# Kernel optimization log

Hardware: AMD Instinct MI355X
Metric: run time of the kernel (lower is better)

## Reference

```python
import jax, jax.numpy as jnp
import numpy as np

N_NODES = 100_000
N_EDGES = 3_200_000
HID = 64


def _glorot(key, shape):
    fan_in, fan_out = shape
    lim = np.sqrt(6.0 / (fan_in + fan_out)).astype(np.float32)
    return jax.random.uniform(key, shape, jnp.float32, -lim, lim)


def setup_inputs() -> dict:
    key = jax.random.key(0)
    ks = jax.random.split(key, 9)
    inp = {
        "vertex_features": jax.random.normal(ks[0], (N_NODES, 6), jnp.float32),
        "edges": jax.random.randint(ks[1], (2, N_EDGES), 0, N_NODES, dtype=jnp.int32),
        "weights": jax.random.uniform(ks[2], (N_EDGES,), jnp.float32),
    }
    dims = [(6, HID), (HID, HID), (HID, HID), (HID, HID), (HID, 1)]
    for i, (din, dout) in enumerate(dims):
        inp[f"W{i+1}"] = _glorot(ks[3 + i], (din, dout))
        inp[f"b{i+1}"] = jnp.zeros((dout,), jnp.float32)
    return inp


def reference(vertex_features, edges, weights, W1, b1, W2, b2, W3, b3, W4, b4, W5, b5):
    n = vertex_features.shape[0]
    row, col = edges[0], edges[1]
    # gcn_norm: add self-loops (weight 1.0), symmetric normalization.
    loop = jnp.arange(n, dtype=edges.dtype)
    row_f = jnp.concatenate([row, loop])   # source nodes
    col_f = jnp.concatenate([col, loop])   # target nodes (aggregation index)
    w_f = jnp.concatenate([weights, jnp.ones((n,), weights.dtype)])
    deg = jax.ops.segment_sum(w_f, col_f, num_segments=n)
    dinv = jnp.where(deg > 0, jax.lax.rsqrt(deg), jnp.zeros_like(deg))
    norm = dinv[row_f] * w_f * dinv[col_f]  # [E+N]

    x = vertex_features
    for W, b in ((W1, b1), (W2, b2), (W3, b3), (W4, b4), (W5, b5)):
        h = x @ W                              # [N, dout]
        msg = h[row_f] * norm[:, None]         # gather + scale, [E+N, dout]
        agg = jax.ops.segment_sum(msg, col_f, num_segments=n)  # scatter-add
        x = jax.nn.sigmoid(agg + b)
    # global_mean_pool with batch=None -> mean over all nodes, shape [1, 1]
    return jnp.mean(x, axis=0, keepdims=True)
```

## Files before the change

### kernel.cpp

```cpp
#include <hip/hip_runtime.h>
#include <hip/hip_fp16.h>
#include <math.h>


__device__ __forceinline__ float sigf(float x) { return 1.0f / (1.0f + expf(-x)); }

__device__ __forceinline__ float2 bf8x2_to_float2(unsigned short v) {
  unsigned int h2 = ((unsigned int)(v & 0xff00u) << 16) | ((unsigned int)(v & 0x00ffu) << 8);
  __half2 h = *reinterpret_cast<__half2*>(&h2);
  return __half22float2(h);
}

__device__ __forceinline__ float q12f(unsigned int q) {
  unsigned short hb = (unsigned short)(q << 3);
  __half h = *reinterpret_cast<__half*>(&hb);
  return __half2float(h);
}

#define RMASK 0xFFFFF
#define SUBS 8
#define TILE_SHIFT 12
#define TILE (1 << TILE_SHIFT)
#define NBMAX 512

__global__ __launch_bounds__(256) void k_count(const int* __restrict__ col,
                                               int* __restrict__ gcnt,
                                               int* __restrict__ gtile, int E, int NB) {
  __shared__ int lc[NBMAX];
  int t = threadIdx.x;
  for (int i = t; i < NB; i += 256) lc[i] = 0;
  __syncthreads();
  int base = blockIdx.x << TILE_SHIFT;
  int sub = blockIdx.x & (SUBS - 1);
  int hi = base + TILE; if (hi > E) hi = E;
  for (int e = base + t; e < hi; e += 256) atomicAdd(&lc[col[e] >> 8], 1);
  __syncthreads();
  size_t gt = (size_t)blockIdx.x * NB;
  for (int i = t; i < NB; i += 256) {
    int c = lc[i];
    gtile[gt + i] = c;
    if (c) atomicAdd(&gcnt[i * SUBS + sub], c);
  }
}

__global__ __launch_bounds__(1024) void k_bscan(const int* __restrict__ gcnt,
                                                int* __restrict__ boff,
                                                int* __restrict__ bnextp,
                                                int* __restrict__ offn, int M, int N) {
  __shared__ int s[1024];
  int t = threadIdx.x;
  int chunk = (M + 1023) / 1024;
  int lo = t * chunk; if (lo > M) lo = M;
  int hi = lo + chunk; if (hi > M) hi = M;
  int sum = 0;
  for (int i = lo; i < hi; ++i) sum += gcnt[i];
  s[t] = sum;
  __syncthreads();
  for (int d = 1; d < 1024; d <<= 1) {
    int v = (t >= d) ? s[t - d] : 0;
    __syncthreads();
    s[t] += v;
    __syncthreads();
  }
  int run = s[t] - sum;
  for (int i = lo; i < hi; ++i) {
    boff[i] = run;
    bnextp[(size_t)i * 16] = run;
    run += gcnt[i];
  }
  if (t == 1023) { boff[M] = s[1023]; offn[N] = s[1023]; }
}

__global__ __launch_bounds__(256) void k_tscatter(const int* __restrict__ row,
                                                  const int* __restrict__ col,
                                                  const float* __restrict__ w,
                                                  const int* __restrict__ gtile,
                                                  int* __restrict__ bnextp,
                                                  int2* __restrict__ raw, int E, int NB) {
  __shared__ int2 buf[TILE];
  __shared__ int loff[NBMAX];
  __shared__ int lc[NBMAX];
  __shared__ int shift[NBMAX];
  __shared__ int sc[256];
  int t = threadIdx.x;
  int e0 = blockIdx.x << TILE_SHIFT;
  int sub = blockIdx.x & (SUBS - 1);
  int e1 = e0 + TILE; if (e1 > E) e1 = E;
  size_t gt = (size_t)blockIdx.x * NB;
  int c0 = (2 * t < NB) ? gtile[gt + 2 * t] : 0;
  int c1 = (2 * t + 1 < NB) ? gtile[gt + 2 * t + 1] : 0;
  sc[t] = c0 + c1;
  __syncthreads();
  for (int d = 1; d < 256; d <<= 1) {
    int v = (t >= d) ? sc[t - d] : 0;
    __syncthreads();
    sc[t] += v;
    __syncthreads();
  }
  int excl = sc[t] - (c0 + c1);
  if (2 * t < NB) { loff[2 * t] = excl; lc[2 * t] = 0; }
  if (2 * t + 1 < NB) { loff[2 * t + 1] = excl + c0; lc[2 * t + 1] = 0; }
  __syncthreads();
  for (int i = t; i < NB; i += 256) {
    int cnt = gtile[gt + i];
    int gb = cnt ? atomicAdd(&bnextp[(size_t)(i * SUBS + sub) * 16], cnt) : 0;
    shift[i] = gb - loff[i];
  }
  __syncthreads();
  for (int e = e0 + t; e < e1; e += 256) {
    int c = col[e];
    int b = c >> 8;
    int pl = loff[b] + atomicAdd(&lc[b], 1);
    unsigned int wh = (unsigned int)__half_as_ushort(__float2half(w[e]));
    buf[pl] = make_int2(row[e] | ((c & 255) << 20), (int)((unsigned)b << 16 | wh));
  }
  __syncthreads();
  int total = e1 - e0;
  for (int i = t; i < total; i += 256) {
    int2 v = buf[i];
    int b = ((unsigned)v.y) >> 16;
    raw[shift[b] + i] = v;
  }
}

__global__ __launch_bounds__(256) void k_bsort(const int2* __restrict__ raw,
                                               const int* __restrict__ boff,
                                               const float* __restrict__ vf,
                                               unsigned int* __restrict__ edat,
                                               int* __restrict__ offn,
                                               float* __restrict__ dinv,
                                               float* __restrict__ vfs, int N) {
  __shared__ int cnt[256];
  __shared__ float wsum[256];
  __shared__ int s[256];
  __shared__ int pos[256];
  __shared__ float dl[256];
  int t = threadIdx.x, b = blockIdx.x;
  int e0 = boff[b * SUBS], e1 = boff[(b + 1) * SUBS];
  cnt[t] = 0;
  wsum[t] = 0.0f;
  __syncthreads();
  for (int e = e0 + t; e < e1; e += 256) {
    int2 a = raw[e];
    int cl = ((unsigned)a.x) >> 20;
    unsigned short wh = (unsigned short)(a.y & 0xffff);
    atomicAdd(&cnt[cl], 1);
    atomicAdd(&wsum[cl], __half2float(*reinterpret_cast<__half*>(&wh)));
  }
  __syncthreads();
  int c = cnt[t];
  s[t] = c;
  __syncthreads();
  for (int d = 1; d < 256; d <<= 1) {
    int v = (t >= d) ? s[t - d] : 0;
    __syncthreads();
    s[t] += v;
    __syncthreads();
  }
  int excl = s[t] - c;
  float dv = rsqrtf(wsum[t] + 1.0f);
  int node = b * 256 + t;
  if (node < N) {
    dinv[node] = dv;
    offn[node] = e0 + excl;
#pragma unroll
    for (int f = 0; f < 6; ++f) vfs[node * 6 + f] = dv * vf[node * 6 + f];
  }
  pos[t] = e0 + excl;
  dl[t] = dv;
  __syncthreads();
  for (int e = e0 + t; e < e1; e += 256) {
    int2 a = raw[e];
    int cl = ((unsigned)a.x) >> 20;
    unsigned short wh = (unsigned short)(a.y & 0xffff);
    float nrm = __half2float(*reinterpret_cast<__half*>(&wh)) * dl[cl];
    unsigned int q = ((unsigned int)__half_as_ushort(__float2half(nrm)) + 4u) >> 3;
    int p = atomicAdd(&pos[cl], 1);
    edat[p] = (unsigned int)(a.x & RMASK) | (q << 20);
  }
}

__global__ __launch_bounds__(256) void k_agg6(const float* __restrict__ vfs,
                                              const float* __restrict__ dinv,
                                              const int* __restrict__ offn,
                                              const unsigned int* __restrict__ edat,
                                              float* __restrict__ Sx, int N) {
  int t = threadIdx.x, g = t >> 3, f = t & 7;
  int node = blockIdx.x * 32 + g;
  if (node >= N) return;
  bool act = f < 6;
  float dc = dinv[node];
  float acc = act ? dc * vfs[node * 6 + f] : 0.0f;
  int e1 = offn[node + 1];
  for (int e = offn[node]; e < e1; ++e) {
    unsigned int a = edat[e];
    if (act) acc += q12f(a >> 20) * vfs[(a & RMASK) * 6 + f];
  }
  if (act) Sx[node * 6 + f] = acc;
}

__global__ __launch_bounds__(256) void k_gemm1(const float* __restrict__ Sx,
                                               const float* __restrict__ W1,
                                               const float* __restrict__ b1,
                                               __half* __restrict__ X, int N) {
  __shared__ float Wl[6 * 64];
  __shared__ float bl[64];
  __shared__ float XT[6 * 65];
  int t = threadIdx.x;
  int n0 = blockIdx.x * 64;
  for (int i = t; i < 384; i += 256) {
    Wl[i] = W1[i];
    int n = i / 6, k = i - n * 6;
    int node = n0 + n;
    XT[k * 65 + n] = (node < N) ? Sx[node * 6 + k] : 0.0f;
  }
  if (t < 64) bl[t] = b1[t];
  __syncthreads();
  int c0 = (t & 15) * 4;
  int nn = (t >> 4) * 4;
  float acc[4][4];
#pragma unroll
  for (int i = 0; i < 4; ++i)
#pragma unroll
    for (int j = 0; j < 4; ++j) acc[i][j] = bl[c0 + j];
#pragma unroll
  for (int k = 0; k < 6; ++k) {
    float4 wv = *(const float4*)&Wl[k * 64 + c0];
    float xv[4];
#pragma unroll
    for (int i = 0; i < 4; ++i) xv[i] = XT[k * 65 + nn + i];
#pragma unroll
    for (int i = 0; i < 4; ++i) {
      acc[i][0] += xv[i] * wv.x;
      acc[i][1] += xv[i] * wv.y;
      acc[i][2] += xv[i] * wv.z;
      acc[i][3] += xv[i] * wv.w;
    }
  }
#pragma unroll
  for (int i = 0; i < 4; ++i) {
    int node = n0 + nn + i;
    if (node < N) {
      __half2* dst = (__half2*)(X + (size_t)node * 64 + c0);
      dst[0] = __floats2half2_rn(sigf(acc[i][0]), sigf(acc[i][1]));
      dst[1] = __floats2half2_rn(sigf(acc[i][2]), sigf(acc[i][3]));
    }
  }
}

__global__ __launch_bounds__(256, 2) void k_gemm64(const __half* __restrict__ Xin,
                                                   const float* __restrict__ W,
                                                   const float* __restrict__ dinv,
                                                   __half* __restrict__ Hout, int N) {
  __shared__ float XT[64 * 65];
  __shared__ float Wl[64 * 64];
  int t = threadIdx.x;
  int n0 = blockIdx.x * 64;
#pragma unroll
  for (int i = 0; i < 4; ++i) {
    int idx = (i * 256 + t) * 4;
    *(float4*)&Wl[idx] = *(const float4*)&W[idx];
  }
#pragma unroll
  for (int i = 0; i < 2; ++i) {
    int idx = (i * 256 + t) * 8;
    int n = idx >> 6, k = idx & 63;
    int node = n0 + n;
    __half2 hv[4];
    if (node < N) {
      const __half2* src = (const __half2*)(Xin + (size_t)node * 64 + k);
      hv[0] = src[0]; hv[1] = src[1]; hv[2] = src[2]; hv[3] = src[3];
    } else {
      hv[0] = hv[1] = hv[2] = hv[3] = __floats2half2_rn(0.f, 0.f);
    }
#pragma unroll
    for (int j = 0; j < 4; ++j) {
      float2 f = __half22float2(hv[j]);
      XT[(k + 2 * j) * 65 + n] = f.x;
      XT[(k + 2 * j + 1) * 65 + n] = f.y;
    }
  }
  __syncthreads();
  int c0 = (t & 15) * 4;
  int nn = (t >> 4) * 4;
  float acc[4][4] = {{0.f}};
#pragma unroll 16
  for (int k = 0; k < 64; ++k) {
    float4 wv = *(const float4*)&Wl[k * 64 + c0];
    float xv[4];
#pragma unroll
    for (int i = 0; i < 4; ++i) xv[i] = XT[k * 65 + nn + i];
#pragma unroll
    for (int i = 0; i < 4; ++i) {
      acc[i][0] += xv[i] * wv.x;
      acc[i][1] += xv[i] * wv.y;
      acc[i][2] += xv[i] * wv.z;
      acc[i][3] += xv[i] * wv.w;
    }
  }
#pragma unroll
  for (int i = 0; i < 4; ++i) {
    int node = n0 + nn + i;
    if (node < N) {
      float dv = dinv[node];
      __half2* dst = (__half2*)(Hout + (size_t)node * 64 + c0);
      dst[0] = __floats2half2_rn(dv * acc[i][0], dv * acc[i][1]);
      dst[1] = __floats2half2_rn(dv * acc[i][2], dv * acc[i][3]);
    }
  }
}

__global__ __launch_bounds__(256) void k_pack(const __half* __restrict__ H,
                                              unsigned char* __restrict__ Hq,
                                              int total8) {
  int i = blockIdx.x * 256 + threadIdx.x;
  if (i >= total8) return;
  uint4 v = ((const uint4*)H)[i];
  unsigned int lo, hi;
  {
    unsigned int a = ((v.x & 0xffffu) + 0x80u) >> 8;
    unsigned int b = (((v.x >> 16) & 0xffffu) + 0x80u) >> 8;
    unsigned int c = ((v.y & 0xffffu) + 0x80u) >> 8;
    unsigned int d = (((v.y >> 16) & 0xffffu) + 0x80u) >> 8;
    lo = (a & 0xffu) | ((b & 0xffu) << 8) | ((c & 0xffu) << 16) | ((d & 0xffu) << 24);
  }
  {
    unsigned int a = ((v.z & 0xffffu) + 0x80u) >> 8;
    unsigned int b = (((v.z >> 16) & 0xffffu) + 0x80u) >> 8;
    unsigned int c = ((v.w & 0xffffu) + 0x80u) >> 8;
    unsigned int d = (((v.w >> 16) & 0xffffu) + 0x80u) >> 8;
    hi = (a & 0xffu) | ((b & 0xffu) << 8) | ((c & 0xffu) << 16) | ((d & 0xffu) << 24);
  }
  ((uint2*)Hq)[i] = make_uint2(lo, hi);
}

template <bool LAST>
__global__ __launch_bounds__(256) void k_agg64(const unsigned char* __restrict__ Hq,
                                               const float* __restrict__ dinv,
                                               const int* __restrict__ offn,
                                               const unsigned int* __restrict__ edat,
                                               const float* __restrict__ b,
                                               const float* __restrict__ W5,
                                               __half* __restrict__ Xout,
                                               float* __restrict__ h5, int N) {
  const unsigned int* Hu = (const unsigned int*)Hq;
  const unsigned int sel0 = 0x01040004u;
  const unsigned int sel1 = 0x03040204u;
  int t = threadIdx.x;
  int l = t & 15;
  int qw = t >> 4;
  int node = blockIdx.x * 16 + qw;
  if (node >= N) return;
  float di = dinv[node];
  unsigned int sh = Hu[(unsigned int)node * 16 + l];
  unsigned int sb0 = __builtin_amdgcn_perm(0u, sh, sel0);
  unsigned int sb1 = __builtin_amdgcn_perm(0u, sh, sel1);
  float2 f01 = __half22float2(*reinterpret_cast<__half2*>(&sb0));
  float2 f23 = __half22float2(*reinterpret_cast<__half2*>(&sb1));
  __half2 acc0 = __floats2half2_rn(di * f01.x, di * f01.y);
  __half2 acc1 = __floats2half2_rn(di * f23.x, di * f23.y);
  int e = offn[node], e1 = offn[node + 1];
  for (; e + 7 < e1; e += 8) {
    unsigned int a[8];
    unsigned int hv[8];
#pragma unroll
    for (int j = 0; j < 8; ++j) a[j] = edat[e + j];
#pragma unroll
    for (int j = 0; j < 8; ++j) hv[j] = Hu[(a[j] & RMASK) * 16u + l];
#pragma unroll
    for (int j = 0; j < 8; ++j) {
      unsigned int nmb = ((a[j] >> 20) << 3) * 0x10001u;
      unsigned int hb0 = __builtin_amdgcn_perm(0u, hv[j], sel0);
      unsigned int hb1 = __builtin_amdgcn_perm(0u, hv[j], sel1);
      acc0 = __hfma2(*reinterpret_cast<__half2*>(&nmb),
                     *reinterpret_cast<__half2*>(&hb0), acc0);
      acc1 = __hfma2(*reinterpret_cast<__half2*>(&nmb),
                     *reinterpret_cast<__half2*>(&hb1), acc1);
    }
  }
  for (; e < e1; ++e) {
    unsigned int a = edat[e];
    unsigned int hv = Hu[(a & RMASK) * 16u + l];
    unsigned int nmb = ((a >> 20) << 3) * 0x10001u;
    unsigned int hb0 = __builtin_amdgcn_perm(0u, hv, sel0);
    unsigned int hb1 = __builtin_amdgcn_perm(0u, hv, sel1);
    acc0 = __hfma2(*reinterpret_cast<__half2*>(&nmb),
                   *reinterpret_cast<__half2*>(&hb0), acc0);
    acc1 = __hfma2(*reinterpret_cast<__half2*>(&nmb),
                   *reinterpret_cast<__half2*>(&hb1), acc1);
  }
  float2 a01 = __half22float2(acc0);
  float2 a23 = __half22float2(acc1);
  float4 bb = ((const float4*)b)[l];
  float x0 = sigf(a01.x + bb.x);
  float x1 = sigf(a01.y + bb.y);
  float x2 = sigf(a23.x + bb.z);
  float x3 = sigf(a23.y + bb.w);
  if (LAST) {
    float4 w5 = ((const float4*)W5)[l];
    float v = x0 * w5.x + x1 * w5.y + x2 * w5.z + x3 * w5.w;
#pragma unroll
    for (int d = 8; d; d >>= 1) v += __shfl_xor(v, d);
    if (l == 0) h5[node] = di * v;
  } else {
    __half2 o0 = __floats2half2_rn(x0, x1);
    __half2 o1 = __floats2half2_rn(x2, x3);
    ((uint2*)(Xout + (size_t)node * 64))[l] =
        make_uint2(*reinterpret_cast<unsigned int*>(&o0),
                   *reinterpret_cast<unsigned int*>(&o1));
  }
}

__global__ __launch_bounds__(256) void k_agg5(const float* __restrict__ h5,
                                              const float* __restrict__ dinv,
                                              const int* __restrict__ offn,
                                              const unsigned int* __restrict__ edat,
                                              const float* __restrict__ b5,
                                              float* __restrict__ partials, int N) {
  int n = blockIdx.x * 256 + threadIdx.x;
  float sig = 0.0f;
  if (n < N) {
    float di = dinv[n];
    float acc = di * h5[n];
    int e1 = offn[n + 1];
    for (int e = offn[n]; e < e1; ++e) {
      unsigned int a = edat[e];
      acc += q12f(a >> 20) * h5[a & RMASK];
    }
    sig = sigf(acc + b5[0]);
  }
#pragma unroll
  for (int d = 32; d; d >>= 1) sig += __shfl_xor(sig, d);
  __shared__ float ws[4];
  int lane = threadIdx.x & 63, wid = threadIdx.x >> 6;
  if (lane == 0) ws[wid] = sig;
  __syncthreads();
  if (threadIdx.x == 0) partials[blockIdx.x] = ws[0] + ws[1] + ws[2] + ws[3];
}

__global__ __launch_bounds__(512) void k_final(const float* __restrict__ partials,
                                               float* __restrict__ out, int nb,
                                               float invN) {
  float v = 0.0f;
  for (int i = threadIdx.x; i < nb; i += 512) v += partials[i];
#pragma unroll
  for (int d = 32; d; d >>= 1) v += __shfl_xor(v, d);
  __shared__ float ws[8];
  int lane = threadIdx.x & 63, wid = threadIdx.x >> 6;
  if (lane == 0) ws[wid] = v;
  __syncthreads();
  if (threadIdx.x == 0) {
    float s = 0.0f;
    for (int i = 0; i < 8; ++i) s += ws[i];
    out[0] = s * invN;
  }
}

extern "C" void kernel_launch(void* const* d_in, const int* in_sizes, int n_in,
                              void* d_out, int out_size, void* d_ws, size_t ws_size,
                              hipStream_t stream) {
  const float* vf = (const float*)d_in[0];
  const int* edges = (const int*)d_in[1];
  const float* w = (const float*)d_in[2];
  const float* W1 = (const float*)d_in[3];
  const float* b1 = (const float*)d_in[4];
  const float* W2 = (const float*)d_in[5];
  const float* b2 = (const float*)d_in[6];
  const float* W3 = (const float*)d_in[7];
  const float* b3 = (const float*)d_in[8];
  const float* W4 = (const float*)d_in[9];
  const float* b4 = (const float*)d_in[10];
  const float* W5 = (const float*)d_in[11];
  const float* b5 = (const float*)d_in[12];
  float* out = (float*)d_out;

  const int N = in_sizes[0] / 6;
  const int E = in_sizes[2];
  const int* row = edges;
  const int* col = edges + E;
  const int NB = (N + 255) >> 8;
  const int M = NB * SUBS;
  const int tiles = (E + TILE - 1) >> TILE_SHIFT;

  size_t o = 0;
  auto carve = [&](size_t bytes) -> void* {
    void* p = (char*)d_ws + o;
    o += (bytes + 255) & ~(size_t)255;
    return p;
  };
  __half* X = (__half*)carve((size_t)N * 64 * 2);
  size_t hbytes = (size_t)N * 64 * 2;
  size_t rbytes = (size_t)E * 8;
  __half* H = (__half*)carve(hbytes > rbytes ? hbytes : rbytes);
  int2* raw = (int2*)H;
  unsigned char* Hq = (unsigned char*)carve((size_t)N * 64);
  unsigned int* edat = (unsigned int*)carve((size_t)E * 4);
  float* Sx = (float*)carve((size_t)N * 6 * 4);
  float* vfs = (float*)carve((size_t)N * 6 * 4);
  float* dinv = (float*)carve((size_t)N * 4);
  int* boff = (int*)carve((size_t)(M + 1) * 4);
  int* bnextp = (int*)carve((size_t)M * 16 * 4);
  int* gcnt = (int*)carve((size_t)M * 4);
  int* gtile = (int*)carve((size_t)tiles * NB * 4);
  int* offn = (int*)carve((size_t)(N + 1) * 4);
  float* h5 = (float*)carve((size_t)N * 4);
  const int nb5 = (N + 255) / 256;
  float* partials = (float*)carve((size_t)nb5 * 4);

  hipMemsetAsync(gcnt, 0, (size_t)M * 4, stream);

  k_count<<<tiles, 256, 0, stream>>>(col, gcnt, gtile, E, NB);
  k_bscan<<<1, 1024, 0, stream>>>(gcnt, boff, bnextp, offn, M, N);
  k_tscatter<<<tiles, 256, 0, stream>>>(row, col, w, gtile, bnextp, raw, E, NB);
  k_bsort<<<NB, 256, 0, stream>>>(raw, boff, vf, edat, offn, dinv, vfs, N);

  k_agg6<<<(N + 31) / 32, 256, 0, stream>>>(vfs, dinv, offn, edat, Sx, N);
  k_gemm1<<<(N + 63) / 64, 256, 0, stream>>>(Sx, W1, b1, X, N);

  const int nbA = (N + 15) / 16;
  const int total8 = N * 8;
  const int pb = (total8 + 255) / 256;
  k_gemm64<<<(N + 63) / 64, 256, 0, stream>>>(X, W2, dinv, H, N);
  k_pack<<<pb, 256, 0, stream>>>(H, Hq, total8);
  k_agg64<false><<<nbA, 256, 0, stream>>>(Hq, dinv, offn, edat, b2, W5, X, h5, N);
  k_gemm64<<<(N + 63) / 64, 256, 0, stream>>>(X, W3, dinv, H, N);
  k_pack<<<pb, 256, 0, stream>>>(H, Hq, total8);
  k_agg64<false><<<nbA, 256, 0, stream>>>(Hq, dinv, offn, edat, b3, W5, X, h5, N);
  k_gemm64<<<(N + 63) / 64, 256, 0, stream>>>(X, W4, dinv, H, N);
  k_pack<<<pb, 256, 0, stream>>>(H, Hq, total8);
  k_agg64<true><<<nbA, 256, 0, stream>>>(Hq, dinv, offn, edat, b4, W5, X, h5, N);

  k_agg5<<<nb5, 256, 0, stream>>>(h5, dinv, offn, edat, b5, partials, N);
  k_final<<<1, 512, 0, stream>>>(partials, out, nb5, 1.0f / (float)N);
}
```

Before: 393.1 us.

## Fuse fp8 packing into gemm64 epilogue and widen bsort blocks to 512 threads

The GEMM epilogue now rounds its fp16 results and packs the high bytes directly into the 8-bit Hq buffer with a byte permute. This removes the separate k_pack launches and the fp16 H round trip through memory in each of the three hidden layers. k_bsort also runs with 512 threads per block so its edge loops take half as many iterations, while the scan still uses 256 threads. The raw buffer no longer shares storage with H, which adds workspace but leaves the rounding unchanged.

```diff
diff --git a/kernel.cpp b/kernel.cpp
--- a/kernel.cpp
+++ b/kernel.cpp
@@ -4,12 +4,6 @@
 
 
 __device__ __forceinline__ float sigf(float x) { return 1.0f / (1.0f + expf(-x)); }
-
-__device__ __forceinline__ float2 bf8x2_to_float2(unsigned short v) {
-  unsigned int h2 = ((unsigned int)(v & 0xff00u) << 16) | ((unsigned int)(v & 0x00ffu) << 8);
-  __half2 h = *reinterpret_cast<__half2*>(&h2);
-  return __half22float2(h);
-}
 
 __device__ __forceinline__ float q12f(unsigned int q) {
   unsigned short hb = (unsigned short)(q << 3);
@@ -123,7 +117,7 @@
   }
 }
 
-__global__ __launch_bounds__(256) void k_bsort(const int2* __restrict__ raw,
+__global__ __launch_bounds__(512) void k_bsort(const int2* __restrict__ raw,
                                                const int* __restrict__ boff,
                                                const float* __restrict__ vf,
                                                unsigned int* __restrict__ edat,
@@ -137,10 +131,9 @@
   __shared__ float dl[256];
   int t = threadIdx.x, b = blockIdx.x;
   int e0 = boff[b * SUBS], e1 = boff[(b + 1) * SUBS];
-  cnt[t] = 0;
-  wsum[t] = 0.0f;
-  __syncthreads();
-  for (int e = e0 + t; e < e1; e += 256) {
+  if (t < 256) { cnt[t] = 0; wsum[t] = 0.0f; }
+  __syncthreads();
+  for (int e = e0 + t; e < e1; e += 512) {
     int2 a = raw[e];
     int cl = ((unsigned)a.x) >> 20;
     unsigned short wh = (unsigned short)(a.y & 0xffff);
@@ -148,28 +141,30 @@
     atomicAdd(&wsum[cl], __half2float(*reinterpret_cast<__half*>(&wh)));
   }
   __syncthreads();
-  int c = cnt[t];
-  s[t] = c;
+  int c = 0;
+  if (t < 256) { c = cnt[t]; s[t] = c; }
   __syncthreads();
   for (int d = 1; d < 256; d <<= 1) {
-    int v = (t >= d) ? s[t - d] : 0;
+    int v = (t < 256 && t >= d) ? s[t - d] : 0;
     __syncthreads();
-    s[t] += v;
+    if (t < 256) s[t] += v;
     __syncthreads();
   }
-  int excl = s[t] - c;
-  float dv = rsqrtf(wsum[t] + 1.0f);
-  int node = b * 256 + t;
-  if (node < N) {
-    dinv[node] = dv;
-    offn[node] = e0 + excl;
-#pragma unroll
-    for (int f = 0; f < 6; ++f) vfs[node * 6 + f] = dv * vf[node * 6 + f];
-  }
-  pos[t] = e0 + excl;
-  dl[t] = dv;
-  __syncthreads();
-  for (int e = e0 + t; e < e1; e += 256) {
+  if (t < 256) {
+    int excl = s[t] - c;
+    float dv = rsqrtf(wsum[t] + 1.0f);
+    int node = b * 256 + t;
+    if (node < N) {
+      dinv[node] = dv;
+      offn[node] = e0 + excl;
+#pragma unroll
+      for (int f = 0; f < 6; ++f) vfs[node * 6 + f] = dv * vf[node * 6 + f];
+    }
+    pos[t] = e0 + excl;
+    dl[t] = dv;
+  }
+  __syncthreads();
+  for (int e = e0 + t; e < e1; e += 512) {
     int2 a = raw[e];
     int cl = ((unsigned)a.x) >> 20;
     unsigned short wh = (unsigned short)(a.y & 0xffff);
@@ -251,7 +246,7 @@
 __global__ __launch_bounds__(256, 2) void k_gemm64(const __half* __restrict__ Xin,
                                                    const float* __restrict__ W,
                                                    const float* __restrict__ dinv,
-                                                   __half* __restrict__ Hout, int N) {
+                                                   unsigned char* __restrict__ Hq, int N) {
   __shared__ float XT[64 * 65];
   __shared__ float Wl[64 * 64];
   int t = threadIdx.x;
@@ -303,35 +298,14 @@
     int node = n0 + nn + i;
     if (node < N) {
       float dv = dinv[node];
-      __half2* dst = (__half2*)(Hout + (size_t)node * 64 + c0);
-      dst[0] = __floats2half2_rn(dv * acc[i][0], dv * acc[i][1]);
-      dst[1] = __floats2half2_rn(dv * acc[i][2], dv * acc[i][3]);
-    }
-  }
-}
-
-__global__ __launch_bounds__(256) void k_pack(const __half* __restrict__ H,
-                                              unsigned char* __restrict__ Hq,
-                                              int total8) {
-  int i = blockIdx.x * 256 + threadIdx.x;
-  if (i >= total8) return;
-  uint4 v = ((const uint4*)H)[i];
-  unsigned int lo, hi;
-  {
-    unsigned int a = ((v.x & 0xffffu) + 0x80u) >> 8;
-    unsigned int b = (((v.x >> 16) & 0xffffu) + 0x80u) >> 8;
-    unsigned int c = ((v.y & 0xffffu) + 0x80u) >> 8;
-    unsigned int d = (((v.y >> 16) & 0xffffu) + 0x80u) >> 8;
-    lo = (a & 0xffu) | ((b & 0xffu) << 8) | ((c & 0xffu) << 16) | ((d & 0xffu) << 24);
-  }
-  {
-    unsigned int a = ((v.z & 0xffffu) + 0x80u) >> 8;
-    unsigned int b = (((v.z >> 16) & 0xffffu) + 0x80u) >> 8;
-    unsigned int c = ((v.w & 0xffffu) + 0x80u) >> 8;
-    unsigned int d = (((v.w >> 16) & 0xffffu) + 0x80u) >> 8;
-    hi = (a & 0xffu) | ((b & 0xffu) << 8) | ((c & 0xffu) << 16) | ((d & 0xffu) << 24);
-  }
-  ((uint2*)Hq)[i] = make_uint2(lo, hi);
+      __half2 h01 = __floats2half2_rn(dv * acc[i][0], dv * acc[i][1]);
+      __half2 h23 = __floats2half2_rn(dv * acc[i][2], dv * acc[i][3]);
+      unsigned int r01 = *reinterpret_cast<unsigned int*>(&h01) + 0x00800080u;
+      unsigned int r23 = *reinterpret_cast<unsigned int*>(&h23) + 0x00800080u;
+      unsigned int packed = __builtin_amdgcn_perm(r23, r01, 0x07050301u);
+      *(unsigned int*)(Hq + (size_t)node * 64 + c0) = packed;
+    }
+  }
 }
 
 template <bool LAST>
@@ -489,10 +463,7 @@
     return p;
   };
   __half* X = (__half*)carve((size_t)N * 64 * 2);
-  size_t hbytes = (size_t)N * 64 * 2;
-  size_t rbytes = (size_t)E * 8;
-  __half* H = (__half*)carve(hbytes > rbytes ? hbytes : rbytes);
-  int2* raw = (int2*)H;
+  int2* raw = (int2*)carve((size_t)E * 8);
   unsigned char* Hq = (unsigned char*)carve((size_t)N * 64);
   unsigned int* edat = (unsigned int*)carve((size_t)E * 4);
   float* Sx = (float*)carve((size_t)N * 6 * 4);
@@ -512,22 +483,17 @@
   k_count<<<tiles, 256, 0, stream>>>(col, gcnt, gtile, E, NB);
   k_bscan<<<1, 1024, 0, stream>>>(gcnt, boff, bnextp, offn, M, N);
   k_tscatter<<<tiles, 256, 0, stream>>>(row, col, w, gtile, bnextp, raw, E, NB);
-  k_bsort<<<NB, 256, 0, stream>>>(raw, boff, vf, edat, offn, dinv, vfs, N);
+  k_bsort<<<NB, 512, 0, stream>>>(raw, boff, vf, edat, offn, dinv, vfs, N);
 
   k_agg6<<<(N + 31) / 32, 256, 0, stream>>>(vfs, dinv, offn, edat, Sx, N);
   k_gemm1<<<(N + 63) / 64, 256, 0, stream>>>(Sx, W1, b1, X, N);
 
   const int nbA = (N + 15) / 16;
-  const int total8 = N * 8;
-  const int pb = (total8 + 255) / 256;
-  k_gemm64<<<(N + 63) / 64, 256, 0, stream>>>(X, W2, dinv, H, N);
-  k_pack<<<pb, 256, 0, stream>>>(H, Hq, total8);
+  k_gemm64<<<(N + 63) / 64, 256, 0, stream>>>(X, W2, dinv, Hq, N);
   k_agg64<false><<<nbA, 256, 0, stream>>>(Hq, dinv, offn, edat, b2, W5, X, h5, N);
-  k_gemm64<<<(N + 63) / 64, 256, 0, stream>>>(X, W3, dinv, H, N);
-  k_pack<<<pb, 256, 0, stream>>>(H, Hq, total8);
+  k_gemm64<<<(N + 63) / 64, 256, 0, stream>>>(X, W3, dinv, Hq, N);
   k_agg64<false><<<nbA, 256, 0, stream>>>(Hq, dinv, offn, edat, b3, W5, X, h5, N);
-  k_gemm64<<<(N + 63) / 64, 256, 0, stream>>>(X, W4, dinv, H, N);
-  k_pack<<<pb, 256, 0, stream>>>(H, Hq, total8);
+  k_gemm64<<<(N + 63) / 64, 256, 0, stream>>>(X, W4, dinv, Hq, N);
   k_agg64<true><<<nbA, 256, 0, stream>>>(Hq, dinv, offn, edat, b4, W5, X, h5, N);
 
   k_agg5<<<nb5, 256, 0, stream>>>(h5, dinv, offn, edat, b5, partials, N);
```

Measured after the change: 382.9 us. 2.6% less time.
